# Kernel tuning notes

Measured on AMD Instinct MI355X. Metric: run time of the kernel, lower is better.

The kernel has to match this reference:

```python
import jax, jax.numpy as jnp
import numpy as np
import math

HEAD_SIZE = 64
WHERE_CONST = -10000.0


def setup_inputs() -> dict:
    key = jax.random.key(0)
    k1, k2, k3 = jax.random.split(key, 3)
    shape = (4, 16, 2048, 64)  # [B, H, S, D]
    q = jax.random.normal(k1, shape, dtype=jnp.float32)
    k = jax.random.normal(k2, shape, dtype=jnp.float32)
    v = jax.random.normal(k3, shape, dtype=jnp.float32)
    return {"q": q, "k": k, "v": v}


def reference(q, k, v):
    # scores: [B, H, Sq, Sk]
    scale = 1.0 / math.sqrt(HEAD_SIZE)
    scores = jnp.einsum('bhqd,bhkd->bhqk', q, k) * scale
    q_len, k_len = q.shape[-2], k.shape[-2]
    causal_mask = jnp.tril(jnp.ones((q_len, k_len), dtype=bool))[None, None]
    scores = jnp.where(causal_mask, scores, WHERE_CONST)
    probs = jax.nn.softmax(scores, axis=-1)
    # dropout rate is 0.0 -> identity
    out = jnp.einsum('bhqk,bhkd->bhqd', probs, v)  # [B, H, S, D]
    out = jnp.swapaxes(out, 1, 2)                  # [B, S, H, D]
    B, S, H, D = out.shape
    return out.reshape(B, S, H * D)
```

## Files before the change

### kernel.cpp

```cpp
#include <hip/hip_runtime.h>
#include <hip/hip_bf16.h>

typedef __bf16 bf16x8_t __attribute__((ext_vector_type(8)));
typedef float  f32x4_t  __attribute__((ext_vector_type(4)));
typedef short  short8_t __attribute__((ext_vector_type(8)));
typedef short  short4_t __attribute__((ext_vector_type(4)));
typedef unsigned short ushort4_t __attribute__((ext_vector_type(4)));

typedef const __attribute__((address_space(1))) unsigned int* gptr_t;
typedef __attribute__((address_space(3))) unsigned int* lptr_t;

#define NB   4
#define NH   16
#define SEQ  2048
#define HD   64
#define BQ   64
#define BKV  64
#define NT   (SEQ / BKV)
#define TILE_SH (BKV * HD)

#define MASK2 (-14426.950408889634f)
#define QSCL  (0.18033688011112042f)

__device__ __forceinline__ int xaddr(int row, int blk) {
    return row * 64 + (((blk ^ row) & 7) << 3);
}

__global__ void __launch_bounds__(256)
prep_kv(const float* __restrict__ kg, const float* __restrict__ vg,
        unsigned short* __restrict__ kimg, unsigned short* __restrict__ vimg) {
    const int t   = blockIdx.x;
    const int bh  = blockIdx.y;
    const int tid = threadIdx.x;
    const int sr  = tid >> 4;
    const int cb  = tid & 15;
    const int d0  = cb * 4;

    const size_t gbase = ((size_t)bh * SEQ + (size_t)t * BKV) * HD;
    const size_t ibase = ((size_t)bh * NT + t) * TILE_SH;

    f32x4_t v4[4];
    #pragma unroll
    for (int i = 0; i < 4; ++i) {
        const int r = 4 * sr + i;
        f32x4_t k4 = *(const f32x4_t*)(kg + gbase + (size_t)r * HD + d0);
        v4[i]      = *(const f32x4_t*)(vg + gbase + (size_t)r * HD + d0);
        ushort4_t kw;
        #pragma unroll
        for (int j = 0; j < 4; ++j) kw[j] = __builtin_bit_cast(unsigned short, (__bf16)k4[j]);
        *(ushort4_t*)&kimg[ibase + xaddr(r, cb >> 1) + (cb & 1) * 4] = kw;
    }
    #pragma unroll
    for (int j = 0; j < 4; ++j) {
        ushort4_t vw;
        #pragma unroll
        for (int i = 0; i < 4; ++i) vw[i] = __builtin_bit_cast(unsigned short, (__bf16)v4[i][j]);
        *(ushort4_t*)&vimg[ibase + xaddr(d0 + j, sr >> 1) + (sr & 1) * 4] = vw;
    }
}

__device__ __forceinline__ void gl16(const unsigned short* g, short* l) {
    __builtin_amdgcn_global_load_lds((gptr_t)g, (lptr_t)l, 16, 0, 0);
}

__global__ void __launch_bounds__(256)
fa_fwd(const float* __restrict__ qg,
       const unsigned short* __restrict__ kimg,
       const unsigned short* __restrict__ vimg,
       float* __restrict__ outg) {
    __shared__ alignas(16) short kv_lds[2][2][TILE_SH];
    __shared__ alignas(16) short p_lds[64 * 64];

    const int tid  = threadIdx.x;
    const int wave = tid >> 6;
    const int lane = tid & 63;
    const int l16  = lane & 15;
    const int quad = lane >> 4;

    const int bh = blockIdx.x;
    const int qt = (int)gridDim.y - 1 - (int)blockIdx.y;
    const int q0 = qt * BQ;

    const float* qp = qg + (size_t)bh * SEQ * HD;
    const unsigned short* kb = kimg + (size_t)bh * NT * TILE_SH;
    const unsigned short* vb = vimg + (size_t)bh * NT * TILE_SH;

    bf16x8_t qf0, qf1;
    {
        const float* qr = qp + (size_t)(q0 + wave * 16 + l16) * HD;
        f32x4_t a0 = *(const f32x4_t*)(qr + quad * 8);
        f32x4_t a1 = *(const f32x4_t*)(qr + quad * 8 + 4);
        f32x4_t a2 = *(const f32x4_t*)(qr + 32 + quad * 8);
        f32x4_t a3 = *(const f32x4_t*)(qr + 32 + quad * 8 + 4);
        #pragma unroll
        for (int j = 0; j < 4; ++j) {
            qf0[j]     = (__bf16)(a0[j] * QSCL);
            qf0[4 + j] = (__bf16)(a1[j] * QSCL);
            qf1[j]     = (__bf16)(a2[j] * QSCL);
            qf1[4 + j] = (__bf16)(a3[j] * QSCL);
        }
    }

    f32x4_t o_acc[4];
    const f32x4_t zero4 = {0.0f, 0.0f, 0.0f, 0.0f};
    #pragma unroll
    for (int c = 0; c < 4; ++c) o_acc[c] = zero4;
    float m_x = MASK2, l_x = 0.0f;

    auto stage = [&](int buf, int t) {
        const unsigned short* kg_ = kb + (size_t)t * TILE_SH;
        const unsigned short* vg_ = vb + (size_t)t * TILE_SH;
        #pragma unroll
        for (int r = 0; r < 2; ++r) {
            const int loff = r * 2048 + wave * 512;
            const int goff = loff + lane * 8;
            gl16(kg_ + goff, &kv_lds[buf][0][loff]);
            gl16(vg_ + goff, &kv_lds[buf][1][loff]);
        }
    };

    const int qloc = wave * 16 + l16;
    const int nt = qt + 1;
    int cur = 0;

    stage(0, 0);

    #pragma unroll 1
    for (int t = 0; t < nt; ++t) {
        __syncthreads();
        if (t + 1 < nt) stage(cur ^ 1, t + 1);

        const short* kt_ = kv_lds[cur][0];
        const short* vt_ = kv_lds[cur][1];

        f32x4_t s_acc[4];
        #pragma unroll
        for (int c = 0; c < 4; ++c) s_acc[c] = zero4;
        __builtin_amdgcn_s_setprio(1);
        #pragma unroll
        for (int c = 0; c < 4; ++c) {
            const int kvrow = c * 16 + l16;
            bf16x8_t kf0 = __builtin_bit_cast(bf16x8_t, *(const short8_t*)&kt_[xaddr(kvrow, quad)]);
            bf16x8_t kf1 = __builtin_bit_cast(bf16x8_t, *(const short8_t*)&kt_[xaddr(kvrow, quad + 4)]);
            s_acc[c] = __builtin_amdgcn_mfma_f32_16x16x32_bf16(kf0, qf0, s_acc[c], 0, 0, 0);
            s_acc[c] = __builtin_amdgcn_mfma_f32_16x16x32_bf16(kf1, qf1, s_acc[c], 0, 0, 0);
        }
        __builtin_amdgcn_s_setprio(0);

        float sv[4][4];
        float vmax = MASK2;
        const bool diag = (t == nt - 1);
        #pragma unroll
        for (int c = 0; c < 4; ++c) {
            #pragma unroll
            for (int r = 0; r < 4; ++r) {
                float x = s_acc[c][r];
                if (diag && (c * 16 + quad * 4 + r > qloc)) x = MASK2;
                sv[c][r] = x;
                vmax = fmaxf(vmax, x);
            }
        }
        vmax = fmaxf(vmax, __shfl_xor(vmax, 16));
        vmax = fmaxf(vmax, __shfl_xor(vmax, 32));

        if (__any((int)(vmax > m_x))) {
            float mn = fmaxf(m_x, vmax);
            float a  = __builtin_amdgcn_exp2f(m_x - mn);
            m_x = mn;
            l_x *= a;
            float ar[4];
            #pragma unroll
            for (int r = 0; r < 4; ++r)
                ar[r] = __shfl(a, (lane & 48) | (quad * 4 + r));
            #pragma unroll
            for (int c = 0; c < 4; ++c)
                #pragma unroll
                for (int r = 0; r < 4; ++r)
                    o_acc[c][r] *= ar[r];
        }

        const int prow = wave * 16 + l16;
        float rs = 0.0f;
        #pragma unroll
        for (int c = 0; c < 4; ++c) {
            short4_t pw;
            #pragma unroll
            for (int r = 0; r < 4; ++r) {
                float p = __builtin_amdgcn_exp2f(sv[c][r] - m_x);
                rs += p;
                pw[r] = __builtin_bit_cast(short, (__bf16)p);
            }
            *(short4_t*)&p_lds[xaddr(prow, 2 * c + (quad >> 1)) + (quad & 1) * 4] = pw;
        }
        rs += __shfl_xor(rs, 16);
        rs += __shfl_xor(rs, 32);
        l_x += rs;


        bf16x8_t pf0 = __builtin_bit_cast(bf16x8_t, *(const short8_t*)&p_lds[xaddr(prow, quad)]);
        bf16x8_t pf1 = __builtin_bit_cast(bf16x8_t, *(const short8_t*)&p_lds[xaddr(prow, quad + 4)]);
        __builtin_amdgcn_s_setprio(1);
        #pragma unroll
        for (int c = 0; c < 4; ++c) {
            const int d = c * 16 + l16;
            bf16x8_t b0 = __builtin_bit_cast(bf16x8_t, *(const short8_t*)&vt_[xaddr(d, quad)]);
            bf16x8_t b1 = __builtin_bit_cast(bf16x8_t, *(const short8_t*)&vt_[xaddr(d, quad + 4)]);
            o_acc[c] = __builtin_amdgcn_mfma_f32_16x16x32_bf16(pf0, b0, o_acc[c], 0, 0, 0);
            o_acc[c] = __builtin_amdgcn_mfma_f32_16x16x32_bf16(pf1, b1, o_acc[c], 0, 0, 0);
        }
        __builtin_amdgcn_s_setprio(0);

        cur ^= 1;
    }

    const int b = bh >> 4;
    const int h = bh & 15;
    #pragma unroll
    for (int r = 0; r < 4; ++r) {
        const float lr = __shfl(l_x, (lane & 48) | (quad * 4 + r));
        const float inv_l = 1.0f / fmaxf(lr, 1e-30f);
        const int row = q0 + wave * 16 + quad * 4 + r;
        float* op = outg + ((size_t)b * SEQ + row) * (NH * HD) + h * HD;
        #pragma unroll
        for (int c = 0; c < 4; ++c) {
            float val = o_acc[c][r] * inv_l;
            unsigned bits = __builtin_bit_cast(unsigned, val);
            if ((bits & 0x7F800000u) == 0x7F800000u) val = 0.0f;
            op[c * 16 + l16] = val;
        }
    }
}

#define LSTR 72
__device__ __forceinline__ int swz(int rowi, int blk) {
    return rowi * LSTR + (((blk) ^ (rowi >> 3)) & 7) * 8;
}

__global__ void __launch_bounds__(256)
fa_fwd_fb(const float* __restrict__ qg,
          const float* __restrict__ kg,
          const float* __restrict__ vg,
          float* __restrict__ outg) {
    __shared__ alignas(16) short k_lds[BKV * LSTR];
    __shared__ alignas(16) short vt_lds[HD * LSTR];
    __shared__ alignas(16) short p_lds2[BQ * LSTR];

    const int tid  = threadIdx.x;
    const int wave = tid >> 6;
    const int lane = tid & 63;
    const int l16  = lane & 15;
    const int quad = lane >> 4;

    const int bh = blockIdx.x;
    const int qt = (int)gridDim.y - 1 - (int)blockIdx.y;
    const int q0 = qt * BQ;

    const size_t base = (size_t)bh * SEQ * HD;
    const float* qp = qg + base;
    const float* kp = kg + base;
    const float* vp = vg + base;

    bf16x8_t qf0, qf1;
    {
        const float* qr = qp + (size_t)(q0 + wave * 16 + l16) * HD;
        f32x4_t a0 = *(const f32x4_t*)(qr + quad * 8);
        f32x4_t a1 = *(const f32x4_t*)(qr + quad * 8 + 4);
        f32x4_t a2 = *(const f32x4_t*)(qr + 32 + quad * 8);
        f32x4_t a3 = *(const f32x4_t*)(qr + 32 + quad * 8 + 4);
        #pragma unroll
        for (int j = 0; j < 4; ++j) {
            qf0[j]     = (__bf16)(a0[j] * QSCL);
            qf0[4 + j] = (__bf16)(a1[j] * QSCL);
            qf1[j]     = (__bf16)(a2[j] * QSCL);
            qf1[4 + j] = (__bf16)(a3[j] * QSCL);
        }
    }

    f32x4_t o_acc[4];
    const f32x4_t zero4 = {0.0f, 0.0f, 0.0f, 0.0f};
    #pragma unroll
    for (int c = 0; c < 4; ++c) o_acc[c] = zero4;
    float m_x = MASK2, l_x = 0.0f;

    const int sr = tid >> 4;
    const int cb = tid & 15;
    const int d0 = cb * 4;
    f32x4_t kreg[4], vreg[4];

    auto issue = [&](int kt0) {
        const float* kr = kp + (size_t)(kt0 + 4 * sr) * HD + d0;
        const float* vr = vp + (size_t)(kt0 + 4 * sr) * HD + d0;
        #pragma unroll
        for (int i = 0; i < 4; ++i) {
            kreg[i] = *(const f32x4_t*)(kr + i * HD);
            vreg[i] = *(const f32x4_t*)(vr + i * HD);
        }
    };
    auto stg = [&]() {
        #pragma unroll
        for (int i = 0; i < 4; ++i) {
            const int r0 = 4 * sr + i;
            short4_t kw;
            #pragma unroll
            for (int j = 0; j < 4; ++j) kw[j] = __builtin_bit_cast(short, (__bf16)kreg[i][j]);
            *(short4_t*)&k_lds[swz(r0, cb >> 1) + (cb & 1) * 4] = kw;
        }
        #pragma unroll
        for (int j = 0; j < 4; ++j) {
            short4_t vw;
            #pragma unroll
            for (int i = 0; i < 4; ++i) vw[i] = __builtin_bit_cast(short, (__bf16)vreg[i][j]);
            *(short4_t*)&vt_lds[swz(d0 + j, sr >> 1) + (sr & 1) * 4] = vw;
        }
    };

    issue(0);
    const int qloc = wave * 16 + l16;
    const int nt = qt + 1;
    for (int t = 0; t < nt; ++t) {
        __syncthreads();
        stg();
        __syncthreads();
        if (t + 1 < nt) issue((t + 1) * BKV);

        f32x4_t s_acc[4];
        #pragma unroll
        for (int c = 0; c < 4; ++c) s_acc[c] = zero4;
        #pragma unroll
        for (int c = 0; c < 4; ++c) {
            const int kvrow = c * 16 + l16;
            bf16x8_t kf0 = __builtin_bit_cast(bf16x8_t, *(const short8_t*)&k_lds[swz(kvrow, quad)]);
            bf16x8_t kf1 = __builtin_bit_cast(bf16x8_t, *(const short8_t*)&k_lds[swz(kvrow, quad + 4)]);
            s_acc[c] = __builtin_amdgcn_mfma_f32_16x16x32_bf16(kf0, qf0, s_acc[c], 0, 0, 0);
            s_acc[c] = __builtin_amdgcn_mfma_f32_16x16x32_bf16(kf1, qf1, s_acc[c], 0, 0, 0);
        }

        float sv[4][4];
        float vmax = MASK2;
        const bool diag = (t == nt - 1);
        #pragma unroll
        for (int c = 0; c < 4; ++c)
            #pragma unroll
            for (int r = 0; r < 4; ++r) {
                float x = s_acc[c][r];
                if (diag && (c * 16 + quad * 4 + r > qloc)) x = MASK2;
                sv[c][r] = x;
                vmax = fmaxf(vmax, x);
            }
        vmax = fmaxf(vmax, __shfl_xor(vmax, 16));
        vmax = fmaxf(vmax, __shfl_xor(vmax, 32));
        if (__any((int)(vmax > m_x))) {
            float mn = fmaxf(m_x, vmax);
            float a  = __builtin_amdgcn_exp2f(m_x - mn);
            m_x = mn;
            l_x *= a;
            float ar[4];
            #pragma unroll
            for (int r = 0; r < 4; ++r) ar[r] = __shfl(a, (lane & 48) | (quad * 4 + r));
            #pragma unroll
            for (int c = 0; c < 4; ++c)
                #pragma unroll
                for (int r = 0; r < 4; ++r) o_acc[c][r] *= ar[r];
        }

        const int prow = wave * 16 + l16;
        float rs = 0.0f;
        #pragma unroll
        for (int c = 0; c < 4; ++c) {
            short4_t pw;
            #pragma unroll
            for (int r = 0; r < 4; ++r) {
                float p = __builtin_amdgcn_exp2f(sv[c][r] - m_x);
                rs += p;
                pw[r] = __builtin_bit_cast(short, (__bf16)p);
            }
            *(short4_t*)&p_lds2[swz(prow, 2 * c + (quad >> 1)) + (quad & 1) * 4] = pw;
        }
        rs += __shfl_xor(rs, 16);
        rs += __shfl_xor(rs, 32);
        l_x += rs;

        bf16x8_t pf0 = __builtin_bit_cast(bf16x8_t, *(const short8_t*)&p_lds2[swz(prow, quad)]);
        bf16x8_t pf1 = __builtin_bit_cast(bf16x8_t, *(const short8_t*)&p_lds2[swz(prow, quad + 4)]);
        #pragma unroll
        for (int c = 0; c < 4; ++c) {
            const int d = c * 16 + l16;
            bf16x8_t b0 = __builtin_bit_cast(bf16x8_t, *(const short8_t*)&vt_lds[swz(d, quad)]);
            bf16x8_t b1 = __builtin_bit_cast(bf16x8_t, *(const short8_t*)&vt_lds[swz(d, quad + 4)]);
            o_acc[c] = __builtin_amdgcn_mfma_f32_16x16x32_bf16(pf0, b0, o_acc[c], 0, 0, 0);
            o_acc[c] = __builtin_amdgcn_mfma_f32_16x16x32_bf16(pf1, b1, o_acc[c], 0, 0, 0);
        }
    }

    const int b = bh >> 4;
    const int h = bh & 15;
    #pragma unroll
    for (int r = 0; r < 4; ++r) {
        const float lr = __shfl(l_x, (lane & 48) | (quad * 4 + r));
        const float inv_l = 1.0f / fmaxf(lr, 1e-30f);
        const int row = q0 + wave * 16 + quad * 4 + r;
        float* op = outg + ((size_t)b * SEQ + row) * (NH * HD) + h * HD;
        #pragma unroll
        for (int c = 0; c < 4; ++c) {
            float val = o_acc[c][r] * inv_l;
            unsigned bits = __builtin_bit_cast(unsigned, val);
            if ((bits & 0x7F800000u) == 0x7F800000u) val = 0.0f;
            op[c * 16 + l16] = val;
        }
    }
}

extern "C" void kernel_launch(void* const* d_in, const int* in_sizes, int n_in,
                              void* d_out, int out_size, void* d_ws, size_t ws_size,
                              hipStream_t stream) {
    const float* q = (const float*)d_in[0];
    const float* k = (const float*)d_in[1];
    const float* v = (const float*)d_in[2];
    float* out = (float*)d_out;

    const size_t img_sh = (size_t)NB * NH * NT * TILE_SH;
    const size_t need   = 2 * img_sh * sizeof(unsigned short);

    if (d_ws != nullptr && ws_size >= need) {
        unsigned short* kimg = (unsigned short*)d_ws;
        unsigned short* vimg = kimg + img_sh;
        prep_kv<<<dim3(NT, NB * NH), 256, 0, stream>>>(k, v, kimg, vimg);
        fa_fwd<<<dim3(NB * NH, SEQ / BQ), 256, 0, stream>>>(q, kimg, vimg, out);
    } else {
        fa_fwd_fb<<<dim3(NB * NH, SEQ / BQ), 256, 0, stream>>>(q, k, v, out);
    }
}
```

Before: 201.2 us.

## Defer online-softmax rescale with threshold, reduce row sums once, stage V transpose in LDS

The attention kernel now rescales the running max only when some lane's local max exceeds the current max by more than a threshold of 8 in log2 units. The cross-lane max reduction moves inside that rare branch, and the per-tile row-sum shuffles are replaced by a single reduction after the loop. This removes shuffles and rescale work from every KV tile, but lets exp2 values grow to about 256 before rescaling, which loosens the overflow margin. Separately, the prep kernel writes the transposed V tile through LDS so it can issue coalesced 16-byte global stores.

```diff
diff --git a/kernel.cpp b/kernel.cpp
--- a/kernel.cpp
+++ b/kernel.cpp
@@ -21,6 +21,7 @@
 
 #define MASK2 (-14426.950408889634f)
 #define QSCL  (0.18033688011112042f)
+#define DEFER_THR 8.0f
 
 __device__ __forceinline__ int xaddr(int row, int blk) {
     return row * 64 + (((blk ^ row) & 7) << 3);
@@ -29,6 +30,8 @@
 __global__ void __launch_bounds__(256)
 prep_kv(const float* __restrict__ kg, const float* __restrict__ vg,
         unsigned short* __restrict__ kimg, unsigned short* __restrict__ vimg) {
+    __shared__ alignas(16) unsigned short vstage[TILE_SH];
+
     const int t   = blockIdx.x;
     const int bh  = blockIdx.y;
     const int tid = threadIdx.x;
@@ -55,8 +58,12 @@
         ushort4_t vw;
         #pragma unroll
         for (int i = 0; i < 4; ++i) vw[i] = __builtin_bit_cast(unsigned short, (__bf16)v4[i][j]);
-        *(ushort4_t*)&vimg[ibase + xaddr(d0 + j, sr >> 1) + (sr & 1) * 4] = vw;
-    }
+        *(ushort4_t*)&vstage[xaddr(d0 + j, sr >> 1) + (sr & 1) * 4] = vw;
+    }
+    __syncthreads();
+    const int s0 = tid * 16;
+    *(short8_t*)&vimg[ibase + s0]     = *(const short8_t*)&vstage[s0];
+    *(short8_t*)&vimg[ibase + s0 + 8] = *(const short8_t*)&vstage[s0 + 8];
 }
 
 __device__ __forceinline__ void gl16(const unsigned short* g, short* l) {
@@ -105,7 +112,8 @@
     const f32x4_t zero4 = {0.0f, 0.0f, 0.0f, 0.0f};
     #pragma unroll
     for (int c = 0; c < 4; ++c) o_acc[c] = zero4;
-    float m_x = MASK2, l_x = 0.0f;
+    float m_x = MASK2;
+    float l_x = 0.0f;
 
     auto stage = [&](int buf, int t) {
         const unsigned short* kg_ = kb + (size_t)t * TILE_SH;
@@ -148,7 +156,6 @@
         __builtin_amdgcn_s_setprio(0);
 
         float sv[4][4];
-        float vmax = MASK2;
         const bool diag = (t == nt - 1);
         #pragma unroll
         for (int c = 0; c < 4; ++c) {
@@ -157,14 +164,19 @@
                 float x = s_acc[c][r];
                 if (diag && (c * 16 + quad * 4 + r > qloc)) x = MASK2;
                 sv[c][r] = x;
-                vmax = fmaxf(vmax, x);
             }
         }
-        vmax = fmaxf(vmax, __shfl_xor(vmax, 16));
-        vmax = fmaxf(vmax, __shfl_xor(vmax, 32));
-
-        if (__any((int)(vmax > m_x))) {
-            float mn = fmaxf(m_x, vmax);
+        float cm[4];
+        #pragma unroll
+        for (int c = 0; c < 4; ++c)
+            cm[c] = fmaxf(fmaxf(sv[c][0], sv[c][1]), fmaxf(sv[c][2], sv[c][3]));
+        const float vloc = fmaxf(fmaxf(cm[0], cm[1]), fmaxf(cm[2], cm[3]));
+
+        if (__any((int)(vloc > m_x + DEFER_THR))) {
+            float vr = vloc;
+            vr = fmaxf(vr, __shfl_xor(vr, 16));
+            vr = fmaxf(vr, __shfl_xor(vr, 32));
+            float mn = fmaxf(m_x, vr);
             float a  = __builtin_amdgcn_exp2f(m_x - mn);
             m_x = mn;
             l_x *= a;
@@ -192,8 +204,6 @@
             }
             *(short4_t*)&p_lds[xaddr(prow, 2 * c + (quad >> 1)) + (quad & 1) * 4] = pw;
         }
-        rs += __shfl_xor(rs, 16);
-        rs += __shfl_xor(rs, 32);
         l_x += rs;
 
 
@@ -213,6 +223,8 @@
         cur ^= 1;
     }
 
+    l_x += __shfl_xor(l_x, 16);
+    l_x += __shfl_xor(l_x, 32);
     const int b = bh >> 4;
     const int h = bh & 15;
     #pragma unroll
```

New measurement: 186.6 us. 1.08x faster.
